# Kernel optimization log

Measured on AMD Instinct MI355X. Metric: run time of the kernel, lower is better.

The kernel has to match this reference:

```python
import jax, jax.numpy as jnp
import numpy as np

D_MODEL = 1024
N_HEADS = 16
D_HEAD = D_MODEL // N_HEADS


def setup_inputs() -> dict:
    key = jax.random.key(0)
    ks = jax.random.split(key, 11)
    B, S = 4, 2048
    scale = 1.0 / np.sqrt(D_MODEL)
    inp = {
        "query": jax.random.normal(ks[0], (B, S, D_MODEL), jnp.float32),
        "key": jax.random.normal(ks[1], (B, S, D_MODEL), jnp.float32),
        "value": jax.random.normal(ks[2], (B, S, D_MODEL), jnp.float32),
        "Wq": jax.random.normal(ks[3], (D_MODEL, D_MODEL), jnp.float32) * scale,
        "bq": jnp.zeros((D_MODEL,), jnp.float32),
        "Wk": jax.random.normal(ks[4], (D_MODEL, D_MODEL), jnp.float32) * scale,
        "bk": jnp.zeros((D_MODEL,), jnp.float32),
        "Wv": jax.random.normal(ks[5], (D_MODEL, D_MODEL), jnp.float32) * scale,
        "bv": jnp.zeros((D_MODEL,), jnp.float32),
        "Wo": jax.random.normal(ks[6], (D_MODEL, D_MODEL), jnp.float32) * scale,
        "bo": jnp.zeros((D_MODEL,), jnp.float32),
    }
    return inp


def _split_heads(x):
    b, s, _ = x.shape
    return x.reshape(b, s, N_HEADS, D_HEAD).transpose(0, 2, 1, 3)  # [b,h,s,dh]


def reference(query, key, value, Wq, bq, Wk, bk, Wv, bv, Wo, bo):
    Q = _split_heads(query @ Wq + bq)
    K = _split_heads(key @ Wk + bk)
    V = _split_heads(value @ Wv + bv)
    scores = jnp.einsum("bhqd,bhkd->bhqk", Q, K) / jnp.sqrt(jnp.float32(D_HEAD))
    attn = jax.nn.softmax(scores, axis=-1)  # dropout p=0 (eval)
    context = jnp.einsum("bhqk,bhkd->bhqd", attn, V)
    b, h, s, dh = context.shape
    context = context.transpose(0, 2, 1, 3).reshape(b, s, D_MODEL)
    return context @ Wo + bo
```

## Files before the change

### kernel.cpp

```cpp
#include <hip/hip_runtime.h>
#include <stdint.h>

#define DM 1024
#define SEQ 2048
#define MTOT 8192

typedef __attribute__((ext_vector_type(8))) short bf16x8;
typedef __attribute__((ext_vector_type(4))) float f32x4;
typedef __attribute__((ext_vector_type(16))) float f32x16;
typedef __attribute__((ext_vector_type(8))) unsigned short u16x8;
typedef __attribute__((ext_vector_type(4))) unsigned short u16x4;
typedef __attribute__((ext_vector_type(4))) uint32_t u32x4;

__device__ __forceinline__ unsigned short f2bf(float x) {
  uint32_t u = __builtin_bit_cast(uint32_t, x);
  u += 0x7fffu + ((u >> 16) & 1u);
  return (unsigned short)(u >> 16);
}

__device__ __forceinline__ uint32_t cvtpk_bf16(float lo, float hi) {
  uint32_t r;
  asm("v_cvt_pk_bf16_f32 %0, %1, %2" : "=v"(r) : "v"(lo), "v"(hi));
  return r;
}

__device__ __forceinline__ void gload16(void* lds, const void* g) {
  __builtin_amdgcn_global_load_lds(
      (const __attribute__((address_space(1))) void*)(uintptr_t)g,
      (__attribute__((address_space(3))) void*)(uintptr_t)lds,
      16, 0, 0);
}

__global__ __launch_bounds__(256)
void prep_w(const float* __restrict__ w0, const float* __restrict__ w1,
            const float* __restrict__ w2, const float* __restrict__ w3,
            unsigned short* __restrict__ Wt) {
  const int z = blockIdx.z;
  const float* W = z == 0 ? w0 : z == 1 ? w1 : z == 2 ? w2 : w3;
  unsigned short* out = Wt + (size_t)z * 1048576;
  __shared__ float tile[32][33];
  const int n0 = blockIdx.x * 32, k0 = blockIdx.y * 32;
  const int tx = threadIdx.x & 31, ty = threadIdx.x >> 5;
#pragma unroll
  for (int j = 0; j < 32; j += 8)
    tile[ty + j][tx] = W[(size_t)(k0 + ty + j) * DM + n0 + tx];
  __syncthreads();
#pragma unroll
  for (int j = 0; j < 32; j += 8)
    out[(size_t)(n0 + ty + j) * DM + k0 + tx] = f2bf(tile[tx][ty + j]);
}

__global__ __launch_bounds__(256)
void cvt_f32_bf16(const float* __restrict__ in, unsigned short* __restrict__ out, int n8) {
  int i = blockIdx.x * 256 + threadIdx.x;
  if (i < n8) {
    f32x4 a = *(const f32x4*)(in + (size_t)i * 8);
    f32x4 b = *(const f32x4*)(in + (size_t)i * 8 + 4);
    u16x8 o;
#pragma unroll
    for (int j = 0; j < 4; ++j) { o[j] = f2bf(a[j]); o[4 + j] = f2bf(b[j]); }
    *(u16x8*)(out + (size_t)i * 8) = o;
  }
}

__global__ __launch_bounds__(256)
void cvt3(const float* __restrict__ q, const float* __restrict__ k,
          const float* __restrict__ v, unsigned short* __restrict__ out) {
  const int z = blockIdx.y;
  const float* in = z == 0 ? q : z == 1 ? k : v;
  unsigned short* o = out + (size_t)z * MTOT * DM;
  int i = blockIdx.x * 256 + threadIdx.x;
  f32x4 a = *(const f32x4*)(in + (size_t)i * 8);
  f32x4 b = *(const f32x4*)(in + (size_t)i * 8 + 4);
  u16x8 ov;
#pragma unroll
  for (int j = 0; j < 4; ++j) { ov[j] = f2bf(a[j]); ov[4 + j] = f2bf(b[j]); }
  *(u16x8*)(o + (size_t)i * 8) = ov;
}

template <int MODE>
__global__ __launch_bounds__(256)
void gemm_bt(const unsigned short* __restrict__ A,
             const unsigned short* __restrict__ Wt,
             const float* __restrict__ bias,
             void* __restrict__ C, float oscale) {
  __shared__ char sA[16384];
  __shared__ char sB[16384];
  const int t = threadIdx.x, wave = t >> 6, lane = t & 63;
  const int m0 = blockIdx.x * 128, n0 = blockIdx.y * 128;
  const int wr = (wave >> 1) * 64, wc = (wave & 1) * 64;
  const int lr = lane & 15, kg = lane >> 4;

  f32x4 acc[4][4];
#pragma unroll
  for (int i = 0; i < 4; ++i)
#pragma unroll
    for (int j = 0; j < 4; ++j) acc[i][j] = (f32x4){0.f, 0.f, 0.f, 0.f};

  for (int kt = 0; kt < 16; ++kt) {
    __syncthreads();
#pragma unroll
    for (int i = 0; i < 4; ++i) {
      int c = wave * 4 + i;
      int row = c * 8 + (lane >> 3);
      int bo = ((lane & 7) * 16) ^ ((row & 7) << 4);
      gload16(&sA[c * 1024], (const char*)(A + (size_t)(m0 + row) * DM + kt * 64) + bo);
      gload16(&sB[c * 1024], (const char*)(Wt + (size_t)(n0 + row) * DM + kt * 64) + bo);
    }
    __syncthreads();
#pragma unroll
    for (int ks = 0; ks < 2; ++ks) {
      bf16x8 afr[4], bfr[4];
#pragma unroll
      for (int j = 0; j < 4; ++j) {
        int mr = wr + j * 16 + lr;
        afr[j] = *(const bf16x8*)&sA[mr * 128 + ((ks * 64 + kg * 16) ^ ((mr & 7) << 4))];
        int nr = wc + j * 16 + lr;
        bfr[j] = *(const bf16x8*)&sB[nr * 128 + ((ks * 64 + kg * 16) ^ ((nr & 7) << 4))];
      }
#pragma unroll
      for (int mi = 0; mi < 4; ++mi)
#pragma unroll
        for (int nj = 0; nj < 4; ++nj)
          acc[mi][nj] = __builtin_amdgcn_mfma_f32_16x16x32_bf16(afr[mi], bfr[nj], acc[mi][nj], 0, 0, 0);
    }
  }
#pragma unroll
  for (int nj = 0; nj < 4; ++nj) {
    int col = n0 + wc + nj * 16 + lr;
    float bv = bias[col];
#pragma unroll
    for (int mi = 0; mi < 4; ++mi) {
      int rowseq = m0 + wr + mi * 16 + kg * 4;
      if (MODE == 2) {
        u16x4 pk;
#pragma unroll
        for (int r = 0; r < 4; ++r) pk[r] = f2bf(acc[mi][nj][r] + bv);
        *(u16x4*)((unsigned short*)C +
                  ((size_t)((rowseq >> 11) << 10) + col) * SEQ + (rowseq & 2047)) = pk;
      } else {
#pragma unroll
        for (int r = 0; r < 4; ++r) {
          float v = (acc[mi][nj][r] + bv) * oscale;
          if (MODE == 1) ((float*)C)[(size_t)(rowseq + r) * DM + col] = v;
          else ((unsigned short*)C)[(size_t)(rowseq + r) * DM + col] = f2bf(v);
        }
      }
    }
  }
}

__global__ __launch_bounds__(256)
void gemm_qkv(const unsigned short* __restrict__ Xall,
              const unsigned short* __restrict__ Wt,
              const float* __restrict__ bq, const float* __restrict__ bk,
              const float* __restrict__ bv,
              unsigned short* __restrict__ Qb, unsigned short* __restrict__ Kb,
              unsigned short* __restrict__ Vt, float qscale) {
  __shared__ char sA[16384];
  __shared__ char sB[16384];
  const int z = blockIdx.z;
  const unsigned short* A = Xall + (size_t)z * MTOT * DM;
  const unsigned short* W = Wt + (size_t)z * 1048576;
  const float* bias = z == 0 ? bq : z == 1 ? bk : bv;
  const int t = threadIdx.x, wave = t >> 6, lane = t & 63;
  const int m0 = blockIdx.x * 128, n0 = blockIdx.y * 128;
  const int wr = (wave >> 1) * 64, wc = (wave & 1) * 64;
  const int lr = lane & 15, kg = lane >> 4;

  f32x4 acc[4][4];
#pragma unroll
  for (int i = 0; i < 4; ++i)
#pragma unroll
    for (int j = 0; j < 4; ++j) acc[i][j] = (f32x4){0.f, 0.f, 0.f, 0.f};

  for (int kt = 0; kt < 16; ++kt) {
    __syncthreads();
#pragma unroll
    for (int i = 0; i < 4; ++i) {
      int c = wave * 4 + i;
      int row = c * 8 + (lane >> 3);
      int bo = ((lane & 7) * 16) ^ ((row & 7) << 4);
      gload16(&sA[c * 1024], (const char*)(A + (size_t)(m0 + row) * DM + kt * 64) + bo);
      gload16(&sB[c * 1024], (const char*)(W + (size_t)(n0 + row) * DM + kt * 64) + bo);
    }
    __syncthreads();
#pragma unroll
    for (int ks = 0; ks < 2; ++ks) {
      bf16x8 afr[4], bfr[4];
#pragma unroll
      for (int j = 0; j < 4; ++j) {
        int mr = wr + j * 16 + lr;
        afr[j] = *(const bf16x8*)&sA[mr * 128 + ((ks * 64 + kg * 16) ^ ((mr & 7) << 4))];
        int nr = wc + j * 16 + lr;
        bfr[j] = *(const bf16x8*)&sB[nr * 128 + ((ks * 64 + kg * 16) ^ ((nr & 7) << 4))];
      }
#pragma unroll
      for (int mi = 0; mi < 4; ++mi)
#pragma unroll
        for (int nj = 0; nj < 4; ++nj)
          acc[mi][nj] = __builtin_amdgcn_mfma_f32_16x16x32_bf16(afr[mi], bfr[nj], acc[mi][nj], 0, 0, 0);
    }
  }
  const float sc = z == 0 ? qscale : 1.0f;
#pragma unroll
  for (int nj = 0; nj < 4; ++nj) {
    int col = n0 + wc + nj * 16 + lr;
    float bvv = bias[col];
#pragma unroll
    for (int mi = 0; mi < 4; ++mi) {
      int rowseq = m0 + wr + mi * 16 + kg * 4;
      if (z == 2) {
        u16x4 pk;
#pragma unroll
        for (int r = 0; r < 4; ++r) pk[r] = f2bf(acc[mi][nj][r] + bvv);
        *(u16x4*)(Vt + ((size_t)((rowseq >> 11) << 10) + col) * SEQ + (rowseq & 2047)) = pk;
      } else {
        unsigned short* out = z == 0 ? Qb : Kb;
#pragma unroll
        for (int r = 0; r < 4; ++r)
          out[(size_t)(rowseq + r) * DM + col] = f2bf((acc[mi][nj][r] + bvv) * sc);
      }
    }
  }
}

__global__ __launch_bounds__(512)
void attn(const unsigned short* __restrict__ Qb,
          const unsigned short* __restrict__ Kb,
          const unsigned short* __restrict__ Vt,
          unsigned short* __restrict__ Ctx) {
  __shared__ char sK[4][8192];
  __shared__ char sV[4][8192];
  const int t = threadIdx.x, wave = t >> 6, lane = t & 63;
  const int l31 = lane & 31, hi = lane >> 5;
  const int bh = blockIdx.x, b = bh >> 4, h = bh & 15;
  const int q0 = blockIdx.y * 512;

  const int srow = wave * 8 + (lane >> 3);
  const int sbo = ((lane & 7) * 16) ^ ((srow & 7) << 4);
  const char* gK = (const char*)Kb + ((size_t)b * SEQ + srow) * (DM * 2) + h * 128 + sbo;
  const char* gV = (const char*)Vt + ((size_t)bh * 64 + srow) * (SEQ * 2) + sbo;

#define STAGE1(buf, kt) do { \
    gload16(&sK[buf][wave * 1024], gK + (size_t)(kt) * 131072); \
    gload16(&sV[buf][wave * 1024], gV + (size_t)(kt) * 128); \
  } while (0)

  bf16x8 qfA[4], qfB[4];
  {
    const unsigned short* qpA = Qb + ((size_t)b * SEQ + q0 + wave * 64 + l31) * DM + h * 64 + hi * 8;
    const unsigned short* qpB = qpA + (size_t)32 * DM;
#pragma unroll
    for (int ks = 0; ks < 4; ++ks) {
      qfA[ks] = *(const bf16x8*)(qpA + ks * 16);
      qfB[ks] = *(const bf16x8*)(qpB + ks * 16);
    }
  }

  f32x16 oA0, oA1, oB0, oB1, mInit;
#pragma unroll
  for (int i = 0; i < 16; ++i) {
    oA0[i] = 0.f; oA1[i] = 0.f; oB0[i] = 0.f; oB1[i] = 0.f; mInit[i] = -12.0f;
  }
  float lA = 0.f, lB = 0.f;

  STAGE1(0, 0);
  STAGE1(1, 1);
  __syncthreads();

  for (int p = 0; p < SEQ / 128; ++p) {
    if (p + 1 < SEQ / 128) {
      const int nt = 2 * p + 2;
      STAGE1(nt & 3, nt);
      STAGE1((nt + 1) & 3, nt + 1);
    }
#pragma unroll
    for (int half = 0; half < 2; ++half) {
      const int buf = 2 * (p & 1) + half;

      f32x16 sA0 = mInit, sA1 = mInit, sB0 = mInit, sB1 = mInit;
      const char* kbase = sK[buf];
      __builtin_amdgcn_s_setprio(1);
#pragma unroll
      for (int ks = 0; ks < 4; ++ks) {
        const int swz = (ks * 32 + hi * 16) ^ ((l31 & 7) << 4);
        bf16x8 kf0 = *(const bf16x8*)(kbase + l31 * 128 + swz);
        bf16x8 kf1 = *(const bf16x8*)(kbase + (32 + l31) * 128 + swz);
        sA0 = __builtin_amdgcn_mfma_f32_32x32x16_bf16(kf0, qfA[ks], sA0, 0, 0, 0);
        sB0 = __builtin_amdgcn_mfma_f32_32x32x16_bf16(kf0, qfB[ks], sB0, 0, 0, 0);
        sA1 = __builtin_amdgcn_mfma_f32_32x32x16_bf16(kf1, qfA[ks], sA1, 0, 0, 0);
        sB1 = __builtin_amdgcn_mfma_f32_32x32x16_bf16(kf1, qfB[ks], sB1, 0, 0, 0);
      }
      __builtin_amdgcn_s_setprio(0);

      {
        float a0 = 0.f, a1 = 0.f, b0 = 0.f, b1 = 0.f;
#pragma unroll
        for (int i = 0; i < 16; i += 2) {
          float pa0 = __builtin_amdgcn_exp2f(sA0[i + 0]); sA0[i + 0] = pa0; a0 += pa0;
          float pa1 = __builtin_amdgcn_exp2f(sA0[i + 1]); sA0[i + 1] = pa1; a1 += pa1;
          float pb0 = __builtin_amdgcn_exp2f(sB0[i + 0]); sB0[i + 0] = pb0; b0 += pb0;
          float pb1 = __builtin_amdgcn_exp2f(sB0[i + 1]); sB0[i + 1] = pb1; b1 += pb1;
        }
#pragma unroll
        for (int i = 0; i < 16; i += 2) {
          float pa0 = __builtin_amdgcn_exp2f(sA1[i + 0]); sA1[i + 0] = pa0; a0 += pa0;
          float pa1 = __builtin_amdgcn_exp2f(sA1[i + 1]); sA1[i + 1] = pa1; a1 += pa1;
          float pb0 = __builtin_amdgcn_exp2f(sB1[i + 0]); sB1[i + 0] = pb0; b0 += pb0;
          float pb1 = __builtin_amdgcn_exp2f(sB1[i + 1]); sB1[i + 1] = pb1; b1 += pb1;
        }
        lA += a0 + a1;
        lB += b0 + b1;
      }

      const char* vbase = sV[buf];
#pragma unroll
      for (int sl = 0; sl < 4; ++sl) {
        const f32x16& spA = (sl < 2) ? sA0 : sA1;
        const f32x16& spB = (sl < 2) ? sB0 : sB1;
        const int s8 = (sl & 1) * 8;
        uint32_t ax0 = cvtpk_bf16(spA[s8 + 0], spA[s8 + 1]);
        uint32_t ax1 = cvtpk_bf16(spA[s8 + 2], spA[s8 + 3]);
        uint32_t ay0 = cvtpk_bf16(spA[s8 + 4], spA[s8 + 5]);
        uint32_t ay1 = cvtpk_bf16(spA[s8 + 6], spA[s8 + 7]);
        uint32_t ax0s = (uint32_t)__shfl_xor((int)ax0, 32);
        uint32_t ax1s = (uint32_t)__shfl_xor((int)ax1, 32);
        uint32_t ay0s = (uint32_t)__shfl_xor((int)ay0, 32);
        uint32_t ay1s = (uint32_t)__shfl_xor((int)ay1, 32);
        u32x4 wvA;
        wvA[0] = hi ? ay0s : ax0;
        wvA[1] = hi ? ay1s : ax1;
        wvA[2] = hi ? ay0 : ax0s;
        wvA[3] = hi ? ay1 : ax1s;
        bf16x8 pfA = __builtin_bit_cast(bf16x8, wvA);
        uint32_t bx0 = cvtpk_bf16(spB[s8 + 0], spB[s8 + 1]);
        uint32_t bx1 = cvtpk_bf16(spB[s8 + 2], spB[s8 + 3]);
        uint32_t by0 = cvtpk_bf16(spB[s8 + 4], spB[s8 + 5]);
        uint32_t by1 = cvtpk_bf16(spB[s8 + 6], spB[s8 + 7]);
        uint32_t bx0s = (uint32_t)__shfl_xor((int)bx0, 32);
        uint32_t bx1s = (uint32_t)__shfl_xor((int)bx1, 32);
        uint32_t by0s = (uint32_t)__shfl_xor((int)by0, 32);
        uint32_t by1s = (uint32_t)__shfl_xor((int)by1, 32);
        u32x4 wvB;
        wvB[0] = hi ? by0s : bx0;
        wvB[1] = hi ? by1s : bx1;
        wvB[2] = hi ? by0 : bx0s;
        wvB[3] = hi ? by1 : bx1s;
        bf16x8 pfB = __builtin_bit_cast(bf16x8, wvB);

        const int swz = (sl * 32 + hi * 16) ^ ((l31 & 7) << 4);
        bf16x8 vf0 = *(const bf16x8*)(vbase + l31 * 128 + swz);
        bf16x8 vf1 = *(const bf16x8*)(vbase + (32 + l31) * 128 + swz);
        __builtin_amdgcn_s_setprio(1);
        oA0 = __builtin_amdgcn_mfma_f32_32x32x16_bf16(vf0, pfA, oA0, 0, 0, 0);
        oB0 = __builtin_amdgcn_mfma_f32_32x32x16_bf16(vf0, pfB, oB0, 0, 0, 0);
        oA1 = __builtin_amdgcn_mfma_f32_32x32x16_bf16(vf1, pfA, oA1, 0, 0, 0);
        oB1 = __builtin_amdgcn_mfma_f32_32x32x16_bf16(vf1, pfB, oB1, 0, 0, 0);
        __builtin_amdgcn_s_setprio(0);
      }
    }
    __syncthreads();
  }
#undef STAGE1

  float ltA = lA + __shfl_xor(lA, 32);
  float ltB = lB + __shfl_xor(lB, 32);
  float invA = 1.0f / ltA, invB = 1.0f / ltB;
  unsigned short* orowA = Ctx + ((size_t)b * SEQ + q0 + wave * 64 + l31) * DM + h * 64;
  unsigned short* orowB = orowA + (size_t)32 * DM;
#pragma unroll
  for (int dt = 0; dt < 2; ++dt) {
    const f32x16& oa = dt ? oA1 : oA0;
    const f32x16& ob = dt ? oB1 : oB0;
#pragma unroll
    for (int rg = 0; rg < 4; ++rg) {
      u16x4 pkA, pkB;
#pragma unroll
      for (int i = 0; i < 4; ++i) {
        pkA[i] = f2bf(oa[rg * 4 + i] * invA);
        pkB[i] = f2bf(ob[rg * 4 + i] * invB);
      }
      *(u16x4*)(orowA + dt * 32 + rg * 8 + hi * 4) = pkA;
      *(u16x4*)(orowB + dt * 32 + rg * 8 + hi * 4) = pkB;
    }
  }
}

extern "C" void kernel_launch(void* const* d_in, const int* in_sizes, int n_in,
                              void* d_out, int out_size, void* d_ws, size_t ws_size,
                              hipStream_t stream) {
  const float* query = (const float*)d_in[0];
  const float* key   = (const float*)d_in[1];
  const float* value = (const float*)d_in[2];
  const float* Wq = (const float*)d_in[3];
  const float* bq = (const float*)d_in[4];
  const float* Wk = (const float*)d_in[5];
  const float* bk = (const float*)d_in[6];
  const float* Wv = (const float*)d_in[7];
  const float* bv = (const float*)d_in[8];
  const float* Wo = (const float*)d_in[9];
  const float* bo = (const float*)d_in[10];

  const float QSCALE = 0.125f * 1.44269504088896340736f;
  char* ws = (char*)d_ws;
  const size_t MB = 1048576;

  prep_w<<<dim3(32, 32, 4), 256, 0, stream>>>(Wq, Wk, Wv, Wo, (unsigned short*)ws);
  unsigned short* Wt = (unsigned short*)ws;

  if (ws_size >= 104 * MB) {
    unsigned short* Xall = (unsigned short*)(ws + 8 * MB);
    unsigned short* Qb   = (unsigned short*)(ws + 56 * MB);
    unsigned short* Kb   = (unsigned short*)(ws + 72 * MB);
    unsigned short* Vt   = (unsigned short*)(ws + 88 * MB);
    unsigned short* Xc   = Xall;

    cvt3<<<dim3(4096, 3), 256, 0, stream>>>(query, key, value, Xall);
    gemm_qkv<<<dim3(64, 8, 3), 256, 0, stream>>>(Xall, Wt, bq, bk, bv,
                                                 Qb, Kb, Vt, QSCALE);
    attn<<<dim3(64, 4), 512, 0, stream>>>(Qb, Kb, Vt, Xc);
    gemm_bt<1><<<dim3(64, 8), 256, 0, stream>>>(Xc, Wt + (size_t)3 * 1048576, bo, d_out, 1.0f);
  } else {
    unsigned short* Qb = (unsigned short*)(ws + 8 * MB);
    unsigned short* Kb = (unsigned short*)(ws + 24 * MB);
    unsigned short* Vt = (unsigned short*)(ws + 40 * MB);
    unsigned short* Xc = (unsigned short*)(ws + 56 * MB);

    cvt_f32_bf16<<<4096, 256, 0, stream>>>(query, Xc, MTOT * DM / 8);
    gemm_bt<0><<<dim3(64, 8), 256, 0, stream>>>(Xc, Wt, bq, Qb, QSCALE);
    cvt_f32_bf16<<<4096, 256, 0, stream>>>(key, Xc, MTOT * DM / 8);
    gemm_bt<0><<<dim3(64, 8), 256, 0, stream>>>(Xc, Wt + (size_t)1048576, bk, Kb, 1.0f);
    cvt_f32_bf16<<<4096, 256, 0, stream>>>(value, Xc, MTOT * DM / 8);
    gemm_bt<2><<<dim3(64, 8), 256, 0, stream>>>(Xc, Wt + (size_t)2 * 1048576, bv, Vt, 1.0f);
    attn<<<dim3(64, 4), 512, 0, stream>>>(Qb, Kb, Vt, Xc);
    gemm_bt<1><<<dim3(64, 8), 256, 0, stream>>>(Xc, Wt + (size_t)3 * 1048576, bo, d_out, 1.0f);
  }
}
```

Before: 200.9 us.

## Fuse fp32-to-bf16 input conversion into QKV GEMM and halve attention block size

Removes the separate cvt3 pass and instead loads fp32 activations directly in the QKV GEMM, converting to bf16 in registers before writing the swizzled tile to LDS. This drops a full write and re-read of three bf16 activation copies through global memory, at the cost of synchronous register-staged loads in place of async gload16 for the A operand. The attention kernel also changes from 512-thread blocks over 512 queries to 256-thread blocks over 256 queries, with each wave staging two K/V rows per load. The grid doubles to 512 blocks to improve occupancy and load balance. The workspace-size fallback path is also removed.

```diff
diff --git a/kernel.cpp b/kernel.cpp
--- a/kernel.cpp
+++ b/kernel.cpp
@@ -48,34 +48,6 @@
 #pragma unroll
   for (int j = 0; j < 32; j += 8)
     out[(size_t)(n0 + ty + j) * DM + k0 + tx] = f2bf(tile[tx][ty + j]);
-}
-
-__global__ __launch_bounds__(256)
-void cvt_f32_bf16(const float* __restrict__ in, unsigned short* __restrict__ out, int n8) {
-  int i = blockIdx.x * 256 + threadIdx.x;
-  if (i < n8) {
-    f32x4 a = *(const f32x4*)(in + (size_t)i * 8);
-    f32x4 b = *(const f32x4*)(in + (size_t)i * 8 + 4);
-    u16x8 o;
-#pragma unroll
-    for (int j = 0; j < 4; ++j) { o[j] = f2bf(a[j]); o[4 + j] = f2bf(b[j]); }
-    *(u16x8*)(out + (size_t)i * 8) = o;
-  }
-}
-
-__global__ __launch_bounds__(256)
-void cvt3(const float* __restrict__ q, const float* __restrict__ k,
-          const float* __restrict__ v, unsigned short* __restrict__ out) {
-  const int z = blockIdx.y;
-  const float* in = z == 0 ? q : z == 1 ? k : v;
-  unsigned short* o = out + (size_t)z * MTOT * DM;
-  int i = blockIdx.x * 256 + threadIdx.x;
-  f32x4 a = *(const f32x4*)(in + (size_t)i * 8);
-  f32x4 b = *(const f32x4*)(in + (size_t)i * 8 + 4);
-  u16x8 ov;
-#pragma unroll
-  for (int j = 0; j < 4; ++j) { ov[j] = f2bf(a[j]); ov[4 + j] = f2bf(b[j]); }
-  *(u16x8*)(o + (size_t)i * 8) = ov;
 }
 
 template <int MODE>
@@ -132,26 +104,19 @@
 #pragma unroll
     for (int mi = 0; mi < 4; ++mi) {
       int rowseq = m0 + wr + mi * 16 + kg * 4;
-      if (MODE == 2) {
-        u16x4 pk;
-#pragma unroll
-        for (int r = 0; r < 4; ++r) pk[r] = f2bf(acc[mi][nj][r] + bv);
-        *(u16x4*)((unsigned short*)C +
-                  ((size_t)((rowseq >> 11) << 10) + col) * SEQ + (rowseq & 2047)) = pk;
-      } else {
-#pragma unroll
-        for (int r = 0; r < 4; ++r) {
-          float v = (acc[mi][nj][r] + bv) * oscale;
-          if (MODE == 1) ((float*)C)[(size_t)(rowseq + r) * DM + col] = v;
-          else ((unsigned short*)C)[(size_t)(rowseq + r) * DM + col] = f2bf(v);
-        }
+#pragma unroll
+      for (int r = 0; r < 4; ++r) {
+        float v = (acc[mi][nj][r] + bv) * oscale;
+        if (MODE == 1) ((float*)C)[(size_t)(rowseq + r) * DM + col] = v;
+        else ((unsigned short*)C)[(size_t)(rowseq + r) * DM + col] = f2bf(v);
       }
     }
   }
 }
 
 __global__ __launch_bounds__(256)
-void gemm_qkv(const unsigned short* __restrict__ Xall,
+void gemm_qkv(const float* __restrict__ Xq, const float* __restrict__ Xk,
+              const float* __restrict__ Xv,
               const unsigned short* __restrict__ Wt,
               const float* __restrict__ bq, const float* __restrict__ bk,
               const float* __restrict__ bv,
@@ -160,7 +125,7 @@
   __shared__ char sA[16384];
   __shared__ char sB[16384];
   const int z = blockIdx.z;
-  const unsigned short* A = Xall + (size_t)z * MTOT * DM;
+  const float* Xf = z == 0 ? Xq : z == 1 ? Xk : Xv;
   const unsigned short* W = Wt + (size_t)z * 1048576;
   const float* bias = z == 0 ? bq : z == 1 ? bk : bv;
   const int t = threadIdx.x, wave = t >> 6, lane = t & 63;
@@ -181,8 +146,20 @@
       int c = wave * 4 + i;
       int row = c * 8 + (lane >> 3);
       int bo = ((lane & 7) * 16) ^ ((row & 7) << 4);
-      gload16(&sA[c * 1024], (const char*)(A + (size_t)(m0 + row) * DM + kt * 64) + bo);
       gload16(&sB[c * 1024], (const char*)(W + (size_t)(n0 + row) * DM + kt * 64) + bo);
+    }
+#pragma unroll
+    for (int i = 0; i < 4; ++i) {
+      int c = wave * 4 + i;
+      int row = c * 8 + (lane >> 3);
+      int colf = ((lane & 7) * 8) ^ ((row & 7) << 3);
+      const float* src = Xf + (size_t)(m0 + row) * DM + kt * 64 + colf;
+      f32x4 a = *(const f32x4*)src;
+      f32x4 b2 = *(const f32x4*)(src + 4);
+      u16x8 pk;
+#pragma unroll
+      for (int j = 0; j < 4; ++j) { pk[j] = f2bf(a[j]); pk[4 + j] = f2bf(b2[j]); }
+      *(u16x8*)&sA[c * 1024 + lane * 16] = pk;
     }
     __syncthreads();
 #pragma unroll
@@ -225,7 +202,7 @@
   }
 }
 
-__global__ __launch_bounds__(512)
+__global__ __launch_bounds__(256)
 void attn(const unsigned short* __restrict__ Qb,
           const unsigned short* __restrict__ Kb,
           const unsigned short* __restrict__ Vt,
@@ -235,16 +212,18 @@
   const int t = threadIdx.x, wave = t >> 6, lane = t & 63;
   const int l31 = lane & 31, hi = lane >> 5;
   const int bh = blockIdx.x, b = bh >> 4, h = bh & 15;
-  const int q0 = blockIdx.y * 512;
-
-  const int srow = wave * 8 + (lane >> 3);
+  const int q0 = blockIdx.y * 256;
+
+  const int srow = wave * 16 + (lane >> 3);
   const int sbo = ((lane & 7) * 16) ^ ((srow & 7) << 4);
   const char* gK = (const char*)Kb + ((size_t)b * SEQ + srow) * (DM * 2) + h * 128 + sbo;
   const char* gV = (const char*)Vt + ((size_t)bh * 64 + srow) * (SEQ * 2) + sbo;
 
 #define STAGE1(buf, kt) do { \
-    gload16(&sK[buf][wave * 1024], gK + (size_t)(kt) * 131072); \
-    gload16(&sV[buf][wave * 1024], gV + (size_t)(kt) * 128); \
+    gload16(&sK[buf][wave * 2048],        gK + (size_t)(kt) * 131072); \
+    gload16(&sK[buf][wave * 2048 + 1024], gK + (size_t)(kt) * 131072 + 16384); \
+    gload16(&sV[buf][wave * 2048],        gV + (size_t)(kt) * 128); \
+    gload16(&sV[buf][wave * 2048 + 1024], gV + (size_t)(kt) * 128 + 32768); \
   } while (0)
 
   bf16x8 qfA[4], qfB[4];
@@ -406,34 +385,18 @@
   char* ws = (char*)d_ws;
   const size_t MB = 1048576;
 
-  prep_w<<<dim3(32, 32, 4), 256, 0, stream>>>(Wq, Wk, Wv, Wo, (unsigned short*)ws);
   unsigned short* Wt = (unsigned short*)ws;
-
-  if (ws_size >= 104 * MB) {
-    unsigned short* Xall = (unsigned short*)(ws + 8 * MB);
-    unsigned short* Qb   = (unsigned short*)(ws + 56 * MB);
-    unsigned short* Kb   = (unsigned short*)(ws + 72 * MB);
-    unsigned short* Vt   = (unsigned short*)(ws + 88 * MB);
-    unsigned short* Xc   = Xall;
-
-    cvt3<<<dim3(4096, 3), 256, 0, stream>>>(query, key, value, Xall);
-    gemm_qkv<<<dim3(64, 8, 3), 256, 0, stream>>>(Xall, Wt, bq, bk, bv,
-                                                 Qb, Kb, Vt, QSCALE);
-    attn<<<dim3(64, 4), 512, 0, stream>>>(Qb, Kb, Vt, Xc);
-    gemm_bt<1><<<dim3(64, 8), 256, 0, stream>>>(Xc, Wt + (size_t)3 * 1048576, bo, d_out, 1.0f);
-  } else {
-    unsigned short* Qb = (unsigned short*)(ws + 8 * MB);
-    unsigned short* Kb = (unsigned short*)(ws + 24 * MB);
-    unsigned short* Vt = (unsigned short*)(ws + 40 * MB);
-    unsigned short* Xc = (unsigned short*)(ws + 56 * MB);
-
-    cvt_f32_bf16<<<4096, 256, 0, stream>>>(query, Xc, MTOT * DM / 8);
-    gemm_bt<0><<<dim3(64, 8), 256, 0, stream>>>(Xc, Wt, bq, Qb, QSCALE);
-    cvt_f32_bf16<<<4096, 256, 0, stream>>>(key, Xc, MTOT * DM / 8);
-    gemm_bt<0><<<dim3(64, 8), 256, 0, stream>>>(Xc, Wt + (size_t)1048576, bk, Kb, 1.0f);
-    cvt_f32_bf16<<<4096, 256, 0, stream>>>(value, Xc, MTOT * DM / 8);
-    gemm_bt<2><<<dim3(64, 8), 256, 0, stream>>>(Xc, Wt + (size_t)2 * 1048576, bv, Vt, 1.0f);
-    attn<<<dim3(64, 4), 512, 0, stream>>>(Qb, Kb, Vt, Xc);
-    gemm_bt<1><<<dim3(64, 8), 256, 0, stream>>>(Xc, Wt + (size_t)3 * 1048576, bo, d_out, 1.0f);
-  }
-}
+  unsigned short* Qb = (unsigned short*)(ws + 8 * MB);
+  unsigned short* Kb = (unsigned short*)(ws + 24 * MB);
+  unsigned short* Vt = (unsigned short*)(ws + 40 * MB);
+  unsigned short* Xc = (unsigned short*)(ws + 56 * MB);
+
+  prep_w<<<dim3(32, 32, 4), 256, 0, stream>>>(Wq, Wk, Wv, Wo, Wt);
+
+  gemm_qkv<<<dim3(64, 8, 3), 256, 0, stream>>>(query, key, value, Wt,
+                                               bq, bk, bv, Qb, Kb, Vt, QSCALE);
+
+  attn<<<dim3(64, 8), 256, 0, stream>>>(Qb, Kb, Vt, Xc);
+
+  gemm_bt<1><<<dim3(64, 8), 256, 0, stream>>>(Xc, Wt + (size_t)3 * 1048576, bo, d_out, 1.0f);
+}
```

New measurement: 234.5 us. +16.7%, slower.
